# Performance work log

Hardware: AMD Instinct MI355X
Metric: run time of the kernel (lower is better)

## Reference

```python
import jax, jax.numpy as jnp
import numpy as np

NUM_HEADS = 32
KV_HEADS = 8
HEAD_DIM = 64
HIDDEN = 2048
ROPE_THETA = 10000.0


def setup_inputs() -> dict:
    key = jax.random.key(0)
    ks = jax.random.split(key, 5)
    B, S, H = 2, 2048, HIDDEN
    scale = 0.02
    return {
        "x": jax.random.normal(ks[0], (B, S, H), dtype=jnp.float32),
        # weights stored as (in_features, out_features)
        "Wq": jax.random.normal(ks[1], (H, NUM_HEADS * HEAD_DIM), dtype=jnp.float32) * scale,
        "Wk": jax.random.normal(ks[2], (H, KV_HEADS * HEAD_DIM), dtype=jnp.float32) * scale,
        "Wv": jax.random.normal(ks[3], (H, KV_HEADS * HEAD_DIM), dtype=jnp.float32) * scale,
        "Wo": jax.random.normal(ks[4], (H, H), dtype=jnp.float32) * scale,
    }


def _rope_tables(seq_len, dtype):
    # freq over even dims, angles concatenated twice -> (S, HEAD_DIM)
    freq = 1.0 / (ROPE_THETA ** (jnp.arange(0, HEAD_DIM, 2, dtype=jnp.float32) / HEAD_DIM))
    ang = jnp.arange(seq_len, dtype=jnp.float32)[:, None] * freq[None, :]
    emb = jnp.concatenate([ang, ang], axis=-1)
    return jnp.cos(emb).astype(dtype), jnp.sin(emb).astype(dtype)


def _rotate_half(x):
    x1, x2 = jnp.split(x, 2, axis=-1)
    return jnp.concatenate([-x2, x1], axis=-1)


def reference(x, Wq, Wk, Wv, Wo):
    B, S, H = x.shape
    q = jnp.einsum("bsd,df->bsf", x, Wq).reshape(B, S, NUM_HEADS, HEAD_DIM).transpose(0, 2, 1, 3)
    k = jnp.einsum("bsd,df->bsf", x, Wk).reshape(B, S, KV_HEADS, HEAD_DIM).transpose(0, 2, 1, 3)
    v = jnp.einsum("bsd,df->bsf", x, Wv).reshape(B, S, KV_HEADS, HEAD_DIM).transpose(0, 2, 1, 3)

    cos, sin = _rope_tables(S, x.dtype)  # (S, HEAD_DIM), broadcasts over (B, h, S, D)
    q = q * cos + _rotate_half(q) * sin
    k = k * cos + _rotate_half(k) * sin

    n_rep = NUM_HEADS // KV_HEADS
    k = jnp.repeat(k, n_rep, axis=1)  # (B, NUM_HEADS, S, D)
    v = jnp.repeat(v, n_rep, axis=1)

    scores = jnp.einsum("bhsd,bhtd->bhst", q, k) / jnp.sqrt(jnp.asarray(HEAD_DIM, x.dtype))
    weights = jax.nn.softmax(scores, axis=-1)
    ctx = jnp.einsum("bhst,bhtd->bhsd", weights, v)
    ctx = ctx.transpose(0, 2, 1, 3).reshape(B, S, H)
    return jnp.einsum("bsd,df->bsf", ctx, Wo)
```

## Files before the change

### kernel.cpp

```cpp
#include <hip/hip_runtime.h>

typedef short s8v __attribute__((ext_vector_type(8)));
typedef int i2v __attribute__((ext_vector_type(2)));
typedef float f2v __attribute__((ext_vector_type(2)));
typedef float f4v __attribute__((ext_vector_type(4)));

typedef const __attribute__((address_space(1))) char* gp1_t;
typedef __attribute__((address_space(3))) char* lp3_t;

__device__ __forceinline__ float bf2f(short s) {
    union { unsigned u; float f; } c;
    c.u = ((unsigned)(unsigned short)s) << 16;
    return c.f;
}
__device__ __forceinline__ short f2bf(float f) {
    union { float f; unsigned u; } c; c.f = f;
    unsigned r = (c.u + 0x7FFFu + ((c.u >> 16) & 1u)) >> 16;
    return (short)r;
}
__device__ __forceinline__ unsigned cvt_pk_bf16(float a, float b) {
    unsigned r;
    asm("v_cvt_pk_bf16_f32 %0, %1, %2" : "=v"(r) : "v"(a), "v"(b));
    return r;
}
__device__ __forceinline__ s8v cvt8(const float* __restrict__ p) {
    f4v a = *(const f4v*)p;
    f4v b = *(const f4v*)(p + 4);
    s8v r;
    r[0] = f2bf(a[0]); r[1] = f2bf(a[1]); r[2] = f2bf(a[2]); r[3] = f2bf(a[3]);
    r[4] = f2bf(b[0]); r[5] = f2bf(b[1]); r[6] = f2bf(b[2]); r[7] = f2bf(b[3]);
    return r;
}


__global__ __launch_bounds__(256) void cvt_x(const float* __restrict__ x,
                                             short* __restrict__ xb) {
    long i = ((long)blockIdx.x * 256 + threadIdx.x) * 8;
    *(s8v*)&xb[i] = cvt8(&x[i]);
}

__global__ __launch_bounds__(256) void cvt_wt(const float* __restrict__ W,
                                              short* __restrict__ Wt,
                                              int N, int obase, float scale) {
    __shared__ __align__(16) short tile[64 * 72];
    const int kt = blockIdx.y * 64, n0 = blockIdx.x * 64;
    const int t = threadIdx.x;
    const int r = t >> 4, c4 = (t & 15) * 4;
#pragma unroll
    for (int i = 0; i < 4; i++) {
        int kr = r + i * 16;
        f4v v = *(const f4v*)&W[(long)(kt + kr) * N + n0 + c4];
#pragma unroll
        for (int j = 0; j < 4; j++) tile[(c4 + j) * 72 + kr] = f2bf(v[j] * scale);
    }
    __syncthreads();
    const int nr = t >> 3, kc = (t & 7) * 8;
#pragma unroll
    for (int i = 0; i < 2; i++) {
        int n = nr + i * 32;
        *(s8v*)&Wt[(long)(obase + n0 + n) * 2048 + kt + kc] = *(const s8v*)&tile[n * 72 + kc];
    }
}

template <bool CF32, bool ROPE>
__global__ __launch_bounds__(512, 2) void gemm_bt8(const short* __restrict__ A,
                                                   const short* __restrict__ Bt,
                                                   void* __restrict__ Cv,
                                                   int K, int lda, int ldb, int ldc) {
    __shared__ __align__(16) short Ab[2][16384];
    __shared__ __align__(16) short Bb[2][16384];

    const int tid = threadIdx.x;
    const int lane = tid & 63;
    const int wave = tid >> 6;
    const int quad = lane >> 4;
    const int l15 = lane & 15;

    const int nwg = gridDim.x * gridDim.y;
    int f = blockIdx.y * gridDim.x + blockIdx.x;
    if ((nwg & 7) == 0) f = (f & 7) * (nwg >> 3) + (f >> 3);
    const int m0 = (f / gridDim.x) * 256;
    const int n0 = (f % gridDim.x) * 256;

    const int wm = (wave >> 2) * 128;
    const int wn = (wave & 3) * 64;

    const int rsub = lane >> 3;
    const int sslot = (lane & 7) ^ rsub;
    const short* aS[2][2];
    const short* bS[2][2];
#pragma unroll
    for (int h = 0; h < 2; h++)
#pragma unroll
        for (int i = 0; i < 2; i++) {
            int row = h * 128 + wave * 16 + i * 8 + rsub;
            aS[h][i] = A  + (long)(m0 + row) * lda + sslot * 8;
            bS[h][i] = Bt + (long)(n0 + row) * ldb + sslot * 8;
        }

    auto stageA = [&](int buf, int h, int kt) {
        char* d = (char*)&Ab[buf][0] + h * 16384 + wave * 2048;
        __builtin_amdgcn_global_load_lds((gp1_t)(aS[h][0] + (long)kt * 64), (lp3_t)d, 16, 0, 0);
        __builtin_amdgcn_global_load_lds((gp1_t)(aS[h][1] + (long)kt * 64), (lp3_t)(d + 1024), 16, 0, 0);
    };
    auto stageB = [&](int buf, int h, int kt) {
        char* d = (char*)&Bb[buf][0] + h * 16384 + wave * 2048;
        __builtin_amdgcn_global_load_lds((gp1_t)(bS[h][0] + (long)kt * 64), (lp3_t)d, 16, 0, 0);
        __builtin_amdgcn_global_load_lds((gp1_t)(bS[h][1] + (long)kt * 64), (lp3_t)(d + 1024), 16, 0, 0);
    };

    const int ks0 = (quad ^ (l15 & 7)) * 8;
    const int ks1 = ks0 ^ 32;

    f4v acc[2][4][2][2];
#pragma unroll
    for (int a = 0; a < 2; a++)
#pragma unroll
        for (int b = 0; b < 4; b++)
#pragma unroll
            for (int c = 0; c < 2; c++)
#pragma unroll
                for (int d = 0; d < 2; d++) acc[a][b][c][d] = (f4v){0.f, 0.f, 0.f, 0.f};

    const int NT = K >> 6;

    stageB(0, 0, 0); stageB(0, 1, 0); stageA(0, 0, 0); stageA(0, 1, 0);
    stageB(1, 0, 1); stageB(1, 1, 1); stageA(1, 0, 1);
    asm volatile("s_waitcnt vmcnt(6)" ::: "memory");
    __builtin_amdgcn_s_barrier();

    for (int t = 0; t < NT; ++t) {
        const short* Ac = &Ab[t & 1][0];
        const short* Bc = &Bb[t & 1][0];
        const int nb = (t + 1) & 1;
        s8v af[4][2], bf0[2][2], bf1[2][2];

#pragma unroll
        for (int mi = 0; mi < 4; mi++) {
            const int row = wm + mi * 16 + l15;
            af[mi][0] = *(const s8v*)&Ac[row * 64 + ks0];
            af[mi][1] = *(const s8v*)&Ac[row * 64 + ks1];
        }
#pragma unroll
        for (int ni = 0; ni < 2; ni++) {
            const int row = wn + ni * 16 + l15;
            bf0[ni][0] = *(const s8v*)&Bc[row * 64 + ks0];
            bf0[ni][1] = *(const s8v*)&Bc[row * 64 + ks1];
        }
        if (t + 1 < NT) stageA(nb, 1, t + 1);
        __builtin_amdgcn_s_setprio(1);
#pragma unroll
        for (int mi = 0; mi < 4; mi++)
#pragma unroll
            for (int ni = 0; ni < 2; ni++) {
                acc[0][mi][0][ni] = __builtin_amdgcn_mfma_f32_16x16x32_bf16(af[mi][0], bf0[ni][0], acc[0][mi][0][ni], 0, 0, 0);
                acc[0][mi][0][ni] = __builtin_amdgcn_mfma_f32_16x16x32_bf16(af[mi][1], bf0[ni][1], acc[0][mi][0][ni], 0, 0, 0);
            }
        __builtin_amdgcn_s_setprio(0);
        __builtin_amdgcn_s_barrier();

#pragma unroll
        for (int ni = 0; ni < 2; ni++) {
            const int row = wn + 32 + ni * 16 + l15;
            bf1[ni][0] = *(const s8v*)&Bc[row * 64 + ks0];
            bf1[ni][1] = *(const s8v*)&Bc[row * 64 + ks1];
        }
        __builtin_amdgcn_s_setprio(1);
#pragma unroll
        for (int mi = 0; mi < 4; mi++)
#pragma unroll
            for (int ni = 0; ni < 2; ni++) {
                acc[0][mi][1][ni] = __builtin_amdgcn_mfma_f32_16x16x32_bf16(af[mi][0], bf1[ni][0], acc[0][mi][1][ni], 0, 0, 0);
                acc[0][mi][1][ni] = __builtin_amdgcn_mfma_f32_16x16x32_bf16(af[mi][1], bf1[ni][1], acc[0][mi][1][ni], 0, 0, 0);
            }
        __builtin_amdgcn_s_setprio(0);
        __builtin_amdgcn_s_barrier();

#pragma unroll
        for (int mi = 0; mi < 4; mi++) {
            const int row = wm + 64 + mi * 16 + l15;
            af[mi][0] = *(const s8v*)&Ac[row * 64 + ks0];
            af[mi][1] = *(const s8v*)&Ac[row * 64 + ks1];
        }
        if (t + 2 < NT) stageB(t & 1, 0, t + 2);
        __builtin_amdgcn_s_setprio(1);
#pragma unroll
        for (int mi = 0; mi < 4; mi++)
#pragma unroll
            for (int ni = 0; ni < 2; ni++) {
                acc[1][mi][0][ni] = __builtin_amdgcn_mfma_f32_16x16x32_bf16(af[mi][0], bf0[ni][0], acc[1][mi][0][ni], 0, 0, 0);
                acc[1][mi][0][ni] = __builtin_amdgcn_mfma_f32_16x16x32_bf16(af[mi][1], bf0[ni][1], acc[1][mi][0][ni], 0, 0, 0);
            }
        __builtin_amdgcn_s_setprio(0);
        __builtin_amdgcn_s_barrier();

        if (t + 2 < NT) { stageB(t & 1, 1, t + 2); stageA(t & 1, 0, t + 2); }
        __builtin_amdgcn_s_setprio(1);
#pragma unroll
        for (int mi = 0; mi < 4; mi++)
#pragma unroll
            for (int ni = 0; ni < 2; ni++) {
                acc[1][mi][1][ni] = __builtin_amdgcn_mfma_f32_16x16x32_bf16(af[mi][0], bf1[ni][0], acc[1][mi][1][ni], 0, 0, 0);
                acc[1][mi][1][ni] = __builtin_amdgcn_mfma_f32_16x16x32_bf16(af[mi][1], bf1[ni][1], acc[1][mi][1][ni], 0, 0, 0);
            }
        __builtin_amdgcn_s_setprio(0);
        if (t + 1 < NT) {
            if (t + 1 == NT - 1) asm volatile("s_waitcnt vmcnt(0)" ::: "memory");
            else                 asm volatile("s_waitcnt vmcnt(6)" ::: "memory");
            __builtin_amdgcn_s_barrier();
        }
    }

    if (ROPE && (n0 + wn) < 2560) {
        const float NLOG = -0.4152410118609203f;
        const float fr0 = exp2f((float)l15 * NLOG);
        const float fr1 = exp2f((float)(16 + l15) * NLOG);
#pragma unroll
        for (int qm = 0; qm < 2; qm++)
#pragma unroll
            for (int mi = 0; mi < 4; mi++)
#pragma unroll
                for (int r = 0; r < 4; r++) {
                    const float s = (float)((m0 + wm + qm * 64 + mi * 16 + quad * 4 + r) & 2047);
#pragma unroll
                    for (int ni = 0; ni < 2; ni++) {
                        float sn, cs;
                        __sincosf(s * (ni ? fr1 : fr0), &sn, &cs);
                        float x1 = acc[qm][mi][0][ni][r];
                        float x2 = acc[qm][mi][1][ni][r];
                        acc[qm][mi][0][ni][r] = x1 * cs - x2 * sn;
                        acc[qm][mi][1][ni][r] = x2 * cs + x1 * sn;
                    }
                }
    }

#pragma unroll
    for (int qm = 0; qm < 2; qm++)
#pragma unroll
        for (int mi = 0; mi < 4; mi++)
#pragma unroll
            for (int qn = 0; qn < 2; qn++)
#pragma unroll
                for (int ni = 0; ni < 2; ni++)
#pragma unroll
                    for (int r = 0; r < 4; r++) {
                        int row = m0 + wm + qm * 64 + mi * 16 + quad * 4 + r;
                        int col = n0 + wn + qn * 32 + ni * 16 + l15;
                        float v = acc[qm][mi][qn][ni][r];
                        if (CF32) ((float*)Cv)[(long)row * ldc + col] = v;
                        else      ((short*)Cv)[(long)row * ldc + col] = f2bf(v);
                    }
}

template <bool CF32>
__global__ __launch_bounds__(512, 2) void gemm_bt2(const short* __restrict__ A,
                                                   const short* __restrict__ Bt,
                                                   void* __restrict__ Cv,
                                                   int K, int lda, int ldb, int ldc) {
    __shared__ __align__(16) short Ab[2][8192];
    __shared__ __align__(16) short Bb[2][16384];

    const int tid = threadIdx.x;
    const int lane = tid & 63;
    const int wave = tid >> 6;
    const int quad = lane >> 4;
    const int l15 = lane & 15;

    const int nwg = gridDim.x * gridDim.y;
    int f = blockIdx.y * gridDim.x + blockIdx.x;
    if ((nwg & 7) == 0) f = (f & 7) * (nwg >> 3) + (f >> 3);
    const int m0 = (f / gridDim.x) * 128;
    const int n0 = (f % gridDim.x) * 256;

    const int wm = (wave >> 2) * 64;
    const int wn = (wave & 3) * 64;

    const int rsub = lane >> 3;
    const int sslot = (lane & 7) ^ rsub;
    const short* aS[2];
    const short* bS[4];
#pragma unroll
    for (int i = 0; i < 2; i++)
        aS[i] = A + (long)(m0 + wave * 16 + i * 8 + rsub) * lda + sslot * 8;
#pragma unroll
    for (int i = 0; i < 4; i++)
        bS[i] = Bt + (long)(n0 + wave * 32 + i * 8 + rsub) * ldb + sslot * 8;

    auto stageA = [&](int buf, int kt) {
        char* d = (char*)&Ab[buf][0] + wave * 2048;
        __builtin_amdgcn_global_load_lds((gp1_t)(aS[0] + (long)kt * 64), (lp3_t)d, 16, 0, 0);
        __builtin_amdgcn_global_load_lds((gp1_t)(aS[1] + (long)kt * 64), (lp3_t)(d + 1024), 16, 0, 0);
    };
    auto stageBh = [&](int buf, int h, int kt) {
        char* d = (char*)&Bb[buf][0] + wave * 4096 + h * 2048;
        __builtin_amdgcn_global_load_lds((gp1_t)(bS[2 * h] + (long)kt * 64), (lp3_t)d, 16, 0, 0);
        __builtin_amdgcn_global_load_lds((gp1_t)(bS[2 * h + 1] + (long)kt * 64), (lp3_t)(d + 1024), 16, 0, 0);
    };

    const int ks0 = (quad ^ (l15 & 7)) * 8;
    const int ks1 = ks0 ^ 32;

    f4v acc[4][2][2];
#pragma unroll
    for (int a = 0; a < 4; a++)
#pragma unroll
        for (int b = 0; b < 2; b++)
#pragma unroll
            for (int c = 0; c < 2; c++) acc[a][b][c] = (f4v){0.f, 0.f, 0.f, 0.f};

    const int NT = K >> 6;

    stageA(0, 0); stageBh(0, 0, 0); stageBh(0, 1, 0);
    stageA(1, 1); stageBh(1, 0, 1); stageBh(1, 1, 1);
    asm volatile("s_waitcnt vmcnt(6)" ::: "memory");
    __builtin_amdgcn_s_barrier();

    for (int t = 0; t < NT; ++t) {
        const short* Ac = &Ab[t & 1][0];
        const short* Bc = &Bb[t & 1][0];
        s8v af01[2][2], af23[2][2], bf0[2][2], bf1[2][2];

#pragma unroll
        for (int mi = 0; mi < 2; mi++) {
            const int row = wm + mi * 16 + l15;
            af01[mi][0] = *(const s8v*)&Ac[row * 64 + ks0];
            af01[mi][1] = *(const s8v*)&Ac[row * 64 + ks1];
        }
#pragma unroll
        for (int ni = 0; ni < 2; ni++) {
            const int row = wn + ni * 16 + l15;
            bf0[ni][0] = *(const s8v*)&Bc[row * 64 + ks0];
            bf0[ni][1] = *(const s8v*)&Bc[row * 64 + ks1];
        }
        __builtin_amdgcn_s_setprio(1);
#pragma unroll
        for (int mi = 0; mi < 2; mi++)
#pragma unroll
            for (int ni = 0; ni < 2; ni++) {
                acc[mi][0][ni] = __builtin_amdgcn_mfma_f32_16x16x32_bf16(af01[mi][0], bf0[ni][0], acc[mi][0][ni], 0, 0, 0);
                acc[mi][0][ni] = __builtin_amdgcn_mfma_f32_16x16x32_bf16(af01[mi][1], bf0[ni][1], acc[mi][0][ni], 0, 0, 0);
            }
        __builtin_amdgcn_s_setprio(0);
        __builtin_amdgcn_s_barrier();

#pragma unroll
        for (int ni = 0; ni < 2; ni++) {
            const int row = wn + 32 + ni * 16 + l15;
            bf1[ni][0] = *(const s8v*)&Bc[row * 64 + ks0];
            bf1[ni][1] = *(const s8v*)&Bc[row * 64 + ks1];
        }
        if (t + 2 < NT) stageBh(t & 1, 0, t + 2);
        __builtin_amdgcn_s_setprio(1);
#pragma unroll
        for (int mi = 0; mi < 2; mi++)
#pragma unroll
            for (int ni = 0; ni < 2; ni++) {
                acc[mi][1][ni] = __builtin_amdgcn_mfma_f32_16x16x32_bf16(af01[mi][0], bf1[ni][0], acc[mi][1][ni], 0, 0, 0);
                acc[mi][1][ni] = __builtin_amdgcn_mfma_f32_16x16x32_bf16(af01[mi][1], bf1[ni][1], acc[mi][1][ni], 0, 0, 0);
            }
        __builtin_amdgcn_s_setprio(0);
        __builtin_amdgcn_s_barrier();

#pragma unroll
        for (int mi = 0; mi < 2; mi++) {
            const int row = wm + 32 + mi * 16 + l15;
            af23[mi][0] = *(const s8v*)&Ac[row * 64 + ks0];
            af23[mi][1] = *(const s8v*)&Ac[row * 64 + ks1];
        }
        if (t + 2 < NT) stageBh(t & 1, 1, t + 2);
        __builtin_amdgcn_s_setprio(1);
#pragma unroll
        for (int mi = 0; mi < 2; mi++)
#pragma unroll
            for (int ni = 0; ni < 2; ni++) {
                acc[2 + mi][0][ni] = __builtin_amdgcn_mfma_f32_16x16x32_bf16(af23[mi][0], bf0[ni][0], acc[2 + mi][0][ni], 0, 0, 0);
                acc[2 + mi][0][ni] = __builtin_amdgcn_mfma_f32_16x16x32_bf16(af23[mi][1], bf0[ni][1], acc[2 + mi][0][ni], 0, 0, 0);
            }
        __builtin_amdgcn_s_setprio(0);
        __builtin_amdgcn_s_barrier();

        if (t + 2 < NT) stageA(t & 1, t + 2);
        __builtin_amdgcn_s_setprio(1);
#pragma unroll
        for (int mi = 0; mi < 2; mi++)
#pragma unroll
            for (int ni = 0; ni < 2; ni++) {
                acc[2 + mi][1][ni] = __builtin_amdgcn_mfma_f32_16x16x32_bf16(af23[mi][0], bf1[ni][0], acc[2 + mi][1][ni], 0, 0, 0);
                acc[2 + mi][1][ni] = __builtin_amdgcn_mfma_f32_16x16x32_bf16(af23[mi][1], bf1[ni][1], acc[2 + mi][1][ni], 0, 0, 0);
            }
        __builtin_amdgcn_s_setprio(0);
        if (t + 1 < NT) {
            if (t + 1 == NT - 1) asm volatile("s_waitcnt vmcnt(0)" ::: "memory");
            else                 asm volatile("s_waitcnt vmcnt(6)" ::: "memory");
            __builtin_amdgcn_s_barrier();
        }
    }

#pragma unroll
    for (int mi = 0; mi < 4; mi++)
#pragma unroll
        for (int qn = 0; qn < 2; qn++)
#pragma unroll
            for (int ni = 0; ni < 2; ni++)
#pragma unroll
                for (int r = 0; r < 4; r++) {
                    int row = m0 + wm + mi * 16 + quad * 4 + r;
                    int col = n0 + wn + qn * 32 + ni * 16 + l15;
                    float v = acc[mi][qn][ni][r];
                    if (CF32) ((float*)Cv)[(long)row * ldc + col] = v;
                    else      ((short*)Cv)[(long)row * ldc + col] = f2bf(v);
                }
}

__global__ __launch_bounds__(256) void rope_kernel(short* __restrict__ qkv) {
    int tid = blockIdx.x * 256 + threadIdx.x;
    int p = tid % 1280;
    int row = tid / 1280;
    int head = p >> 5;
    int j = p & 31;
    int s = row & 2047;
    int c1 = head * 64 + j;
    float freq = exp2f(-(float)j * 0.4152410118609203f);
    float ang = (float)s * freq;
    float sn, cs;
    __sincosf(ang, &sn, &cs);
    long base = (long)row * 3072;
    float x1 = bf2f(qkv[base + c1]);
    float x2 = bf2f(qkv[base + c1 + 32]);
    qkv[base + c1]      = f2bf(x1 * cs - x2 * sn);
    qkv[base + c1 + 32] = f2bf(x2 * cs + x1 * sn);
}

__global__ __launch_bounds__(256) void vtrans(const short* __restrict__ qkv,
                                              short* __restrict__ Vt_g) {
    __shared__ __align__(16) short tile[64 * 72];
    const int kt = blockIdx.x * 64;
    const int kvh = blockIdx.y;
    const int b = blockIdx.z;
    const int t = threadIdx.x;
#pragma unroll
    for (int cc = 0; cc < 2; cc++) {
        int ch = t + cc * 256;
        int key = ch >> 3, d0 = (ch & 7) * 8;
        s8v v = *(const s8v*)&qkv[(long)(b * 2048 + kt + key) * 3072 + 2560 + kvh * 64 + d0];
#pragma unroll
        for (int i = 0; i < 8; i++) tile[(d0 + i) * 72 + key] = v[i];
    }
    __syncthreads();
#pragma unroll
    for (int cc = 0; cc < 2; cc++) {
        int ch = t + cc * 256;
        int d = ch >> 3, kc = (ch & 7) * 8;
        *(s8v*)&Vt_g[(long)((b * 8 + kvh) * 64 + d) * 2048 + kt + kc] = *(const s8v*)&tile[d * 72 + kc];
    }
}

__global__ __launch_bounds__(256, 3) void attn4(short* __restrict__ qkv,
                                                const short* __restrict__ Vt_g) {
    __shared__ __align__(16) short KV[2][2][4096];
    __shared__ __align__(16) short Ps[4][2][16 * 72];
    __shared__ float rsb[4][32];

    const int tid = threadIdx.x;
    const int lane = tid & 63;
    const int wave = tid >> 6;
    const int quad = lane >> 4;
    const int l15 = lane & 15;

    int f = (blockIdx.z * 32 + blockIdx.y) * 16 + blockIdx.x;
    f = (f & 7) * 128 + (f >> 3);
    const int b = f >> 9;
    const int h = (f >> 4) & 31;
    const int kvh = h >> 2;
    const int q0 = (f & 15) * 128;

    const long kbase = ((long)b * 2048) * 3072 + 2048 + kvh * 64;
    const long vtbase = (long)(b * 8 + kvh) * 64 * 2048;

    const long qrow = (long)b * 2048 + q0 + wave * 32 + l15;
    const short* qp = qkv + qrow * 3072 + h * 64 + quad * 8;
    const s8v qf00 = *(const s8v*)(qp);
    const s8v qf01 = *(const s8v*)(qp + 32);
    const s8v qf10 = *(const s8v*)(qp + 16 * 3072);
    const s8v qf11 = *(const s8v*)(qp + 16 * 3072 + 32);

    const int rA = wave * 8 + (lane >> 3);
    const int sslot = (lane & 7) ^ (lane >> 3);
    const short* kA = qkv + kbase + (long)rA * 3072 + sslot * 8;
    const short* kB = kA + (long)32 * 3072;
    const short* vA = Vt_g + vtbase + (long)rA * 2048 + sslot * 8;
    const short* vB = vA + (long)32 * 2048;

    {
        char* kd = (char*)&KV[0][0][0] + wave * 1024;
        char* vd = (char*)&KV[0][1][0] + wave * 1024;
        __builtin_amdgcn_global_load_lds((gp1_t)kA, (lp3_t)kd, 16, 0, 0);
        __builtin_amdgcn_global_load_lds((gp1_t)kB, (lp3_t)(kd + 4096), 16, 0, 0);
        __builtin_amdgcn_global_load_lds((gp1_t)vA, (lp3_t)vd, 16, 0, 0);
        __builtin_amdgcn_global_load_lds((gp1_t)vB, (lp3_t)(vd + 4096), 16, 0, 0);
    }
    __syncthreads();

    const int ks0 = ((quad ^ (l15 & 7)) << 3);
    const int ks1 = ks0 ^ 32;

    f2v rs0v = (f2v){0.f, 0.f}, rs1v = (f2v){0.f, 0.f};
    f4v o0[4], o1[4];
#pragma unroll
    for (int ni = 0; ni < 4; ni++) { o0[ni] = (f4v){0.f, 0.f, 0.f, 0.f}; o1[ni] = (f4v){0.f, 0.f, 0.f, 0.f}; }

    short* Pw0 = &Ps[wave][0][0];
    short* Pw1 = &Ps[wave][1][0];

    for (int t = 0; t < 32; ++t) {
        const short* Kb = &KV[t & 1][0][0];
        const short* Vb = &KV[t & 1][1][0];

        if (t < 31) {
            const long ko = (long)(t + 1) * (64 * 3072);
            const long vo = (long)(t + 1) * 64;
            char* kd = (char*)&KV[(t + 1) & 1][0][0] + wave * 1024;
            char* vd = (char*)&KV[(t + 1) & 1][1][0] + wave * 1024;
            __builtin_amdgcn_global_load_lds((gp1_t)(kA + ko), (lp3_t)kd, 16, 0, 0);
            __builtin_amdgcn_global_load_lds((gp1_t)(kB + ko), (lp3_t)(kd + 4096), 16, 0, 0);
            __builtin_amdgcn_global_load_lds((gp1_t)(vA + vo), (lp3_t)vd, 16, 0, 0);
            __builtin_amdgcn_global_load_lds((gp1_t)(vB + vo), (lp3_t)(vd + 4096), 16, 0, 0);
        }

#pragma unroll
        for (int ni = 0; ni < 4; ni++) {
            const int ro = (ni * 16 + l15) * 64;
            const s8v kf0 = *(const s8v*)&Kb[ro + ks0];
            const s8v kf1 = *(const s8v*)&Kb[ro + ks1];
            f4v a = (f4v){-24.f, -24.f, -24.f, -24.f};
            a = __builtin_amdgcn_mfma_f32_16x16x32_bf16(kf0, qf00, a, 0, 0, 0);
            a = __builtin_amdgcn_mfma_f32_16x16x32_bf16(kf1, qf01, a, 0, 0, 0);
            {
                float p0 = exp2f(a[0]);
                float p1 = exp2f(a[1]);
                float p2 = exp2f(a[2]);
                float p3 = exp2f(a[3]);
                rs0v += (f2v){p0, p1};
                rs0v += (f2v){p2, p3};
                *(i2v*)&Pw0[l15 * 72 + ni * 16 + quad * 4] =
                    (i2v){(int)cvt_pk_bf16(p0, p1), (int)cvt_pk_bf16(p2, p3)};
            }
            f4v c = (f4v){-24.f, -24.f, -24.f, -24.f};
            c = __builtin_amdgcn_mfma_f32_16x16x32_bf16(kf0, qf10, c, 0, 0, 0);
            c = __builtin_amdgcn_mfma_f32_16x16x32_bf16(kf1, qf11, c, 0, 0, 0);
            {
                float p0 = exp2f(c[0]);
                float p1 = exp2f(c[1]);
                float p2 = exp2f(c[2]);
                float p3 = exp2f(c[3]);
                rs1v += (f2v){p0, p1};
                rs1v += (f2v){p2, p3};
                *(i2v*)&Pw1[l15 * 72 + ni * 16 + quad * 4] =
                    (i2v){(int)cvt_pk_bf16(p0, p1), (int)cvt_pk_bf16(p2, p3)};
            }
        }

        const s8v pf00 = *(const s8v*)&Pw0[l15 * 72 + quad * 8];
        const s8v pf01 = *(const s8v*)&Pw0[l15 * 72 + 32 + quad * 8];
        const s8v pf10 = *(const s8v*)&Pw1[l15 * 72 + quad * 8];
        const s8v pf11 = *(const s8v*)&Pw1[l15 * 72 + 32 + quad * 8];
#pragma unroll
        for (int ni = 0; ni < 4; ni++) {
            const int ro = (ni * 16 + l15) * 64;
            const s8v vf0 = *(const s8v*)&Vb[ro + ks0];
            const s8v vf1 = *(const s8v*)&Vb[ro + ks1];
            o0[ni] = __builtin_amdgcn_mfma_f32_16x16x32_bf16(pf00, vf0, o0[ni], 0, 0, 0);
            o0[ni] = __builtin_amdgcn_mfma_f32_16x16x32_bf16(pf01, vf1, o0[ni], 0, 0, 0);
            o1[ni] = __builtin_amdgcn_mfma_f32_16x16x32_bf16(pf10, vf0, o1[ni], 0, 0, 0);
            o1[ni] = __builtin_amdgcn_mfma_f32_16x16x32_bf16(pf11, vf1, o1[ni], 0, 0, 0);
        }
        __syncthreads();
    }

    float rs0 = rs0v[0] + rs0v[1];
    float rs1 = rs1v[0] + rs1v[1];
    rs0 += __shfl_xor(rs0, 16); rs0 += __shfl_xor(rs0, 32);
    rs1 += __shfl_xor(rs1, 16); rs1 += __shfl_xor(rs1, 32);
    if (quad == 0) { rsb[wave][l15] = rs0; rsb[wave][16 + l15] = rs1; }
    __syncthreads();

#pragma unroll
    for (int r = 0; r < 4; r++) {
        const float i0 = 1.0f / rsb[wave][quad * 4 + r];
        const float i1 = 1.0f / rsb[wave][16 + quad * 4 + r];
        const long ob0 = ((long)b * 2048 + q0 + wave * 32 + quad * 4 + r) * 3072 + h * 64;
        const long ob1 = ob0 + 16 * 3072;
#pragma unroll
        for (int ni = 0; ni < 4; ni++) {
            qkv[ob0 + ni * 16 + l15] = f2bf(o0[ni][r] * i0);
            qkv[ob1 + ni * 16 + l15] = f2bf(o1[ni][r] * i1);
        }
    }
}


template <bool AF32, bool CF32>
__global__ __launch_bounds__(256) void gemm_bn(const void* __restrict__ Av,
                                               const float* __restrict__ B,
                                               void* __restrict__ Cv,
                                               int K, int N, int lda, int ldc) {
    __shared__ __align__(16) short As[128 * 40];
    __shared__ __align__(16) short Bs[128 * 40];
    const int tid = threadIdx.x;
    const int lane = tid & 63;
    const int wave = tid >> 6;
    const int quad = lane >> 4;
    const int l15 = lane & 15;
    const int m0 = blockIdx.y * 128;
    const int n0 = blockIdx.x * 128;
    const int wm = (wave & 1) * 64;
    const int wn = (wave >> 1) * 64;

    f4v acc[4][4];
#pragma unroll
    for (int i = 0; i < 4; i++)
#pragma unroll
        for (int j = 0; j < 4; j++) acc[i][j] = (f4v){0.f, 0.f, 0.f, 0.f};

    const int ar0 = tid >> 2, akc0 = (tid & 3) * 8;
    const int ar1 = (tid + 256) >> 2, akc1 = ((tid + 256) & 3) * 8;
    const int bk0 = tid >> 4, bnc0 = (tid & 15) * 8;
    const int bk1 = (tid + 256) >> 4, bnc1 = ((tid + 256) & 15) * 8;

    for (int k0 = 0; k0 < K; k0 += 32) {
        __syncthreads();
        if (AF32) {
            const float* A = (const float*)Av;
            *(s8v*)(&As[ar0 * 40 + akc0]) = cvt8(&A[(long)(m0 + ar0) * lda + k0 + akc0]);
            *(s8v*)(&As[ar1 * 40 + akc1]) = cvt8(&A[(long)(m0 + ar1) * lda + k0 + akc1]);
        } else {
            const short* A = (const short*)Av;
            *(s8v*)(&As[ar0 * 40 + akc0]) = *(const s8v*)(&A[(long)(m0 + ar0) * lda + k0 + akc0]);
            *(s8v*)(&As[ar1 * 40 + akc1]) = *(const s8v*)(&A[(long)(m0 + ar1) * lda + k0 + akc1]);
        }
        s8v b0 = cvt8(&B[(long)(k0 + bk0) * N + n0 + bnc0]);
        s8v b1 = cvt8(&B[(long)(k0 + bk1) * N + n0 + bnc1]);
#pragma unroll
        for (int i = 0; i < 8; i++) Bs[(bnc0 + i) * 40 + bk0] = b0[i];
#pragma unroll
        for (int i = 0; i < 8; i++) Bs[(bnc1 + i) * 40 + bk1] = b1[i];
        __syncthreads();
        s8v af[4], bfr[4];
#pragma unroll
        for (int mi = 0; mi < 4; mi++)
            af[mi] = *(const s8v*)(&As[(wm + mi * 16 + l15) * 40 + quad * 8]);
#pragma unroll
        for (int ni = 0; ni < 4; ni++)
            bfr[ni] = *(const s8v*)(&Bs[(wn + ni * 16 + l15) * 40 + quad * 8]);
#pragma unroll
        for (int mi = 0; mi < 4; mi++)
#pragma unroll
            for (int ni = 0; ni < 4; ni++)
                acc[mi][ni] = __builtin_amdgcn_mfma_f32_16x16x32_bf16(af[mi], bfr[ni], acc[mi][ni], 0, 0, 0);
    }
#pragma unroll
    for (int mi = 0; mi < 4; mi++)
#pragma unroll
        for (int ni = 0; ni < 4; ni++)
#pragma unroll
            for (int r = 0; r < 4; r++) {
                int row = m0 + wm + mi * 16 + quad * 4 + r;
                int col = n0 + wn + ni * 16 + l15;
                if (CF32) ((float*)Cv)[(long)row * ldc + col] = acc[mi][ni][r];
                else      ((short*)Cv)[(long)row * ldc + col] = f2bf(acc[mi][ni][r]);
            }
}

__global__ __launch_bounds__(256) void attn_kernel(short* __restrict__ qkv) {
    __shared__ __align__(16) short Qs[64 * 72];
    __shared__ __align__(16) short Ks[64 * 72];
    __shared__ __align__(16) short Vt[64 * 72];
    __shared__ __align__(16) short Ps[4][16 * 72];

    const int tid = threadIdx.x;
    const int lane = tid & 63;
    const int wave = tid >> 6;
    const int quad = lane >> 4;
    const int l15 = lane & 15;
    const int b = blockIdx.z;
    const int h = blockIdx.y;
    const int kvh = h >> 2;
    const int q0 = blockIdx.x * 64;

    const long qbase = ((long)b * 2048 + q0) * 3072 + h * 64;
    const long kbase = ((long)b * 2048) * 3072 + 2048 + kvh * 64;
    const long vbase = kbase + 512;

#pragma unroll
    for (int cc = 0; cc < 2; cc++) {
        int ch = tid + cc * 256;
        int r = ch >> 3, d0 = (ch & 7) * 8;
        *(s8v*)(&Qs[r * 72 + d0]) = *(const s8v*)(&qkv[qbase + (long)r * 3072 + d0]);
    }
    __syncthreads();
    s8v qf[2];
    qf[0] = *(const s8v*)(&Qs[(wave * 16 + l15) * 72 + quad * 8]);
    qf[1] = *(const s8v*)(&Qs[(wave * 16 + l15) * 72 + 32 + quad * 8]);

    float m_i[4], l_i[4];
    f4v o[4];
#pragma unroll
    for (int r = 0; r < 4; r++) { m_i[r] = -1e30f; l_i[r] = 0.0f; }
#pragma unroll
    for (int ni = 0; ni < 4; ni++) o[ni] = (f4v){0.f, 0.f, 0.f, 0.f};

    for (int kt = 0; kt < 2048; kt += 64) {
        __syncthreads();
#pragma unroll
        for (int cc = 0; cc < 2; cc++) {
            int ch = tid + cc * 256;
            int r = ch >> 3, d0 = (ch & 7) * 8;
            *(s8v*)(&Ks[r * 72 + d0]) = *(const s8v*)(&qkv[kbase + (long)(kt + r) * 3072 + d0]);
            s8v v = *(const s8v*)(&qkv[vbase + (long)(kt + r) * 3072 + d0]);
            int g = d0 >> 3;
            int chn = ((r >> 3) ^ g) * 8 + (r & 7);
#pragma unroll
            for (int i = 0; i < 8; i++) Vt[(d0 + i) * 72 + chn] = v[i];
        }
        __syncthreads();

        f4v sc[4];
#pragma unroll
        for (int ni = 0; ni < 4; ni++) {
            s8v kf0 = *(const s8v*)(&Ks[(ni * 16 + l15) * 72 + quad * 8]);
            s8v kf1 = *(const s8v*)(&Ks[(ni * 16 + l15) * 72 + 32 + quad * 8]);
            f4v a = (f4v){0.f, 0.f, 0.f, 0.f};
            a = __builtin_amdgcn_mfma_f32_16x16x32_bf16(qf[0], kf0, a, 0, 0, 0);
            a = __builtin_amdgcn_mfma_f32_16x16x32_bf16(qf[1], kf1, a, 0, 0, 0);
            sc[ni] = a * 0.125f;
        }
        float alpha[4], rs[4];
#pragma unroll
        for (int r = 0; r < 4; r++) {
            float v = fmaxf(fmaxf(sc[0][r], sc[1][r]), fmaxf(sc[2][r], sc[3][r]));
            v = fmaxf(v, __shfl_xor(v, 1));
            v = fmaxf(v, __shfl_xor(v, 2));
            v = fmaxf(v, __shfl_xor(v, 4));
            v = fmaxf(v, __shfl_xor(v, 8));
            float mn = fmaxf(m_i[r], v);
            alpha[r] = __expf(m_i[r] - mn);
            m_i[r] = mn;
            rs[r] = 0.f;
        }
#pragma unroll
        for (int ni = 0; ni < 4; ni++)
#pragma unroll
            for (int r = 0; r < 4; r++) {
                float pv = __expf(sc[ni][r] - m_i[r]);
                sc[ni][r] = pv;
                rs[r] += pv;
            }
#pragma unroll
        for (int r = 0; r < 4; r++) {
            float v = rs[r];
            v += __shfl_xor(v, 1);
            v += __shfl_xor(v, 2);
            v += __shfl_xor(v, 4);
            v += __shfl_xor(v, 8);
            l_i[r] = l_i[r] * alpha[r] + v;
        }
#pragma unroll
        for (int ni = 0; ni < 4; ni++)
#pragma unroll
            for (int r = 0; r < 4; r++) {
                int row = quad * 4 + r;
                int key = ni * 16 + l15;
                int chn = ((key >> 3) ^ (row >> 3)) * 8 + (key & 7);
                Ps[wave][row * 72 + chn] = f2bf(sc[ni][r]);
            }
        __syncthreads();
#pragma unroll
        for (int ni = 0; ni < 4; ni++) {
            f4v t = o[ni];
            t[0] *= alpha[0]; t[1] *= alpha[1]; t[2] *= alpha[2]; t[3] *= alpha[3];
            o[ni] = t;
        }
        s8v pf0 = *(const s8v*)(&Ps[wave][l15 * 72 + ((quad ^ (l15 >> 3)) * 8)]);
        s8v pf1 = *(const s8v*)(&Ps[wave][l15 * 72 + (((4 + quad) ^ (l15 >> 3)) * 8)]);
#pragma unroll
        for (int ni = 0; ni < 4; ni++) {
            int d = ni * 16 + l15;
            s8v vf0 = *(const s8v*)(&Vt[d * 72 + ((quad ^ (d >> 3)) * 8)]);
            s8v vf1 = *(const s8v*)(&Vt[d * 72 + (((4 + quad) ^ (d >> 3)) * 8)]);
            o[ni] = __builtin_amdgcn_mfma_f32_16x16x32_bf16(pf0, vf0, o[ni], 0, 0, 0);
            o[ni] = __builtin_amdgcn_mfma_f32_16x16x32_bf16(pf1, vf1, o[ni], 0, 0, 0);
        }
    }
#pragma unroll
    for (int r = 0; r < 4; r++) {
        float inv = 1.0f / l_i[r];
        int srow = q0 + wave * 16 + quad * 4 + r;
        long obase = ((long)b * 2048 + srow) * 3072 + h * 64;
#pragma unroll
        for (int ni = 0; ni < 4; ni++)
            qkv[obase + ni * 16 + l15] = f2bf(o[ni][r] * inv);
    }
}

extern "C" void kernel_launch(void* const* d_in, const int* in_sizes, int n_in,
                              void* d_out, int out_size, void* d_ws, size_t ws_size,
                              hipStream_t stream) {
    (void)in_sizes; (void)n_in; (void)out_size;
    const float* x  = (const float*)d_in[0];
    const float* Wq = (const float*)d_in[1];
    const float* Wk = (const float*)d_in[2];
    const float* Wv = (const float*)d_in[3];
    const float* Wo = (const float*)d_in[4];

    const float CS = 0.18033688011112042f;
    const size_t need = 67108864ULL;
    if (ws_size >= need) {
        short* xb    = (short*)d_ws;
        short* Wqkvt = xb + 8388608;
        short* Wot   = Wqkvt + 6291456;
        short* qkv   = Wot + 4194304;
        short* Vt_g  = qkv + 12582912;

        cvt_x<<<4096, 256, 0, stream>>>(x, xb);
        cvt_wt<<<dim3(32, 32), 256, 0, stream>>>(Wq, Wqkvt, 2048, 0, 1.0f);
        cvt_wt<<<dim3(8, 32), 256, 0, stream>>>(Wk, Wqkvt, 512, 2048, CS);
        cvt_wt<<<dim3(8, 32), 256, 0, stream>>>(Wv, Wqkvt, 512, 2560, 1.0f);
        cvt_wt<<<dim3(32, 32), 256, 0, stream>>>(Wo, Wot, 2048, 0, 1.0f);
        gemm_bt8<false, true><<<dim3(12, 16), 512, 0, stream>>>(xb, Wqkvt, qkv, 2048, 2048, 2048, 3072);
        vtrans<<<dim3(32, 8, 2), 256, 0, stream>>>(qkv, Vt_g);
        attn4<<<dim3(16, 32, 2), 256, 0, stream>>>(qkv, Vt_g);
        gemm_bt2<true><<<dim3(8, 32), 512, 0, stream>>>(qkv, Wot, d_out, 2048, 3072, 2048, 2048);
    } else {
        short* qkv = (short*)d_ws;
        gemm_bn<true, false><<<dim3(16, 32), 256, 0, stream>>>(x, Wq, qkv,        2048, 2048, 2048, 3072);
        gemm_bn<true, false><<<dim3(4, 32), 256, 0, stream>>>(x, Wk, qkv + 2048, 2048,  512, 2048, 3072);
        gemm_bn<true, false><<<dim3(4, 32), 256, 0, stream>>>(x, Wv, qkv + 2560, 2048,  512, 2048, 3072);
        rope_kernel<<<dim3(20480), 256, 0, stream>>>(qkv);
        attn_kernel<<<dim3(32, 32, 2), 256, 0, stream>>>(qkv);
        gemm_bn<false, true><<<dim3(16, 32), 256, 0, stream>>>(qkv, Wo, d_out, 2048, 2048, 3072, 2048);
    }
}
```

Measured before the change: 333.5 us.

## Keep softmax P in registers by permuting V transpose key order

The attention kernel no longer writes the bf16 probability tile to LDS and reads it back as MFMA A-operands. Instead the packed P values are assembled directly in registers. The V-transpose kernel permutes the key ordering so the register layout of P matches the PV MFMA operand layout. Removing the Ps shared buffer also lowers LDS use, and launch bounds are raised to 4 blocks per CU for more occupancy, at the risk of register pressure.

```diff
diff --git a/kernel.cpp b/kernel.cpp
--- a/kernel.cpp
+++ b/kernel.cpp
@@ -1,6 +1,8 @@
 #include <hip/hip_runtime.h>
 
 typedef short s8v __attribute__((ext_vector_type(8)));
+typedef short s4v __attribute__((ext_vector_type(4)));
+typedef unsigned u4v __attribute__((ext_vector_type(4)));
 typedef int i2v __attribute__((ext_vector_type(2)));
 typedef float f2v __attribute__((ext_vector_type(2)));
 typedef float f4v __attribute__((ext_vector_type(4)));
@@ -450,15 +452,20 @@
 #pragma unroll
     for (int cc = 0; cc < 2; cc++) {
         int ch = t + cc * 256;
-        int d = ch >> 3, kc = (ch & 7) * 8;
-        *(s8v*)&Vt_g[(long)((b * 8 + kvh) * 64 + d) * 2048 + kt + kc] = *(const s8v*)&tile[d * 72 + kc];
-    }
-}
-
-__global__ __launch_bounds__(256, 3) void attn4(short* __restrict__ qkv,
+        int d = ch >> 3, c = ch & 7;
+        int base1 = 32 * (c >> 2) + 4 * (c & 3);
+        s4v lo = *(const s4v*)&tile[d * 72 + base1];
+        s4v hi = *(const s4v*)&tile[d * 72 + base1 + 16];
+        s8v w;
+        w[0] = lo[0]; w[1] = lo[1]; w[2] = lo[2]; w[3] = lo[3];
+        w[4] = hi[0]; w[5] = hi[1]; w[6] = hi[2]; w[7] = hi[3];
+        *(s8v*)&Vt_g[(long)((b * 8 + kvh) * 64 + d) * 2048 + kt + c * 8] = w;
+    }
+}
+
+__global__ __launch_bounds__(256, 4) void attn5(short* __restrict__ qkv,
                                                 const short* __restrict__ Vt_g) {
     __shared__ __align__(16) short KV[2][2][4096];
-    __shared__ __align__(16) short Ps[4][2][16 * 72];
     __shared__ float rsb[4][32];
 
     const int tid = threadIdx.x;
@@ -508,9 +515,6 @@
     f4v o0[4], o1[4];
 #pragma unroll
     for (int ni = 0; ni < 4; ni++) { o0[ni] = (f4v){0.f, 0.f, 0.f, 0.f}; o1[ni] = (f4v){0.f, 0.f, 0.f, 0.f}; }
-
-    short* Pw0 = &Ps[wave][0][0];
-    short* Pw1 = &Ps[wave][1][0];
 
     for (int t = 0; t < 32; ++t) {
         const short* Kb = &KV[t & 1][0][0];
@@ -527,6 +531,7 @@
             __builtin_amdgcn_global_load_lds((gp1_t)(vB + vo), (lp3_t)(vd + 4096), 16, 0, 0);
         }
 
+        unsigned pk0[4][2], pk1[4][2];
 #pragma unroll
         for (int ni = 0; ni < 4; ni++) {
             const int ro = (ni * 16 + l15) * 64;
@@ -542,8 +547,8 @@
                 float p3 = exp2f(a[3]);
                 rs0v += (f2v){p0, p1};
                 rs0v += (f2v){p2, p3};
-                *(i2v*)&Pw0[l15 * 72 + ni * 16 + quad * 4] =
-                    (i2v){(int)cvt_pk_bf16(p0, p1), (int)cvt_pk_bf16(p2, p3)};
+                pk0[ni][0] = cvt_pk_bf16(p0, p1);
+                pk0[ni][1] = cvt_pk_bf16(p2, p3);
             }
             f4v c = (f4v){-24.f, -24.f, -24.f, -24.f};
             c = __builtin_amdgcn_mfma_f32_16x16x32_bf16(kf0, qf10, c, 0, 0, 0);
@@ -555,24 +560,27 @@
                 float p3 = exp2f(c[3]);
                 rs1v += (f2v){p0, p1};
                 rs1v += (f2v){p2, p3};
-                *(i2v*)&Pw1[l15 * 72 + ni * 16 + quad * 4] =
-                    (i2v){(int)cvt_pk_bf16(p0, p1), (int)cvt_pk_bf16(p2, p3)};
-            }
-        }
-
-        const s8v pf00 = *(const s8v*)&Pw0[l15 * 72 + quad * 8];
-        const s8v pf01 = *(const s8v*)&Pw0[l15 * 72 + 32 + quad * 8];
-        const s8v pf10 = *(const s8v*)&Pw1[l15 * 72 + quad * 8];
-        const s8v pf11 = *(const s8v*)&Pw1[l15 * 72 + 32 + quad * 8];
+                pk1[ni][0] = cvt_pk_bf16(p0, p1);
+                pk1[ni][1] = cvt_pk_bf16(p2, p3);
+            }
+        }
+
+        union PU { u4v u; s8v s; };
+        PU pa0, pa1, pb0, pb1;
+        pa0.u = (u4v){pk0[0][0], pk0[0][1], pk0[1][0], pk0[1][1]};
+        pa1.u = (u4v){pk0[2][0], pk0[2][1], pk0[3][0], pk0[3][1]};
+        pb0.u = (u4v){pk1[0][0], pk1[0][1], pk1[1][0], pk1[1][1]};
+        pb1.u = (u4v){pk1[2][0], pk1[2][1], pk1[3][0], pk1[3][1]};
+
 #pragma unroll
         for (int ni = 0; ni < 4; ni++) {
             const int ro = (ni * 16 + l15) * 64;
             const s8v vf0 = *(const s8v*)&Vb[ro + ks0];
             const s8v vf1 = *(const s8v*)&Vb[ro + ks1];
-            o0[ni] = __builtin_amdgcn_mfma_f32_16x16x32_bf16(pf00, vf0, o0[ni], 0, 0, 0);
-            o0[ni] = __builtin_amdgcn_mfma_f32_16x16x32_bf16(pf01, vf1, o0[ni], 0, 0, 0);
-            o1[ni] = __builtin_amdgcn_mfma_f32_16x16x32_bf16(pf10, vf0, o1[ni], 0, 0, 0);
-            o1[ni] = __builtin_amdgcn_mfma_f32_16x16x32_bf16(pf11, vf1, o1[ni], 0, 0, 0);
+            o0[ni] = __builtin_amdgcn_mfma_f32_16x16x32_bf16(pa0.s, vf0, o0[ni], 0, 0, 0);
+            o0[ni] = __builtin_amdgcn_mfma_f32_16x16x32_bf16(pa1.s, vf1, o0[ni], 0, 0, 0);
+            o1[ni] = __builtin_amdgcn_mfma_f32_16x16x32_bf16(pb0.s, vf0, o1[ni], 0, 0, 0);
+            o1[ni] = __builtin_amdgcn_mfma_f32_16x16x32_bf16(pb1.s, vf1, o1[ni], 0, 0, 0);
         }
         __syncthreads();
     }
@@ -828,7 +836,7 @@
         cvt_wt<<<dim3(32, 32), 256, 0, stream>>>(Wo, Wot, 2048, 0, 1.0f);
         gemm_bt8<false, true><<<dim3(12, 16), 512, 0, stream>>>(xb, Wqkvt, qkv, 2048, 2048, 2048, 3072);
         vtrans<<<dim3(32, 8, 2), 256, 0, stream>>>(qkv, Vt_g);
-        attn4<<<dim3(16, 32, 2), 256, 0, stream>>>(qkv, Vt_g);
+        attn5<<<dim3(16, 32, 2), 256, 0, stream>>>(qkv, Vt_g);
         gemm_bt2<true><<<dim3(8, 32), 512, 0, stream>>>(qkv, Wot, d_out, 2048, 3072, 2048, 2048);
     } else {
         short* qkv = (short*)d_ws;
```

Measured after the change: 314.8 us. 5.6% less time.
